# Performance work log

Measured on AMD Instinct MI355X. Metric: run time of the kernel, lower is better.

The kernel has to match this reference:

```python
import jax, jax.numpy as jnp
import numpy as np

C = 0.01          # curvature
EPS = 1e-6        # eps used in midpoint / weight normalization (matches torch code)
MIN_NORM = 1e-10  # numerical floor for norms
BALL_EPS = 1e-5   # projection margin


def _norm(x):
    return jnp.sqrt(jnp.clip(jnp.sum(x * x, axis=-1, keepdims=True), MIN_NORM))


def log_map_zero(x, c):
    sc = jnp.sqrt(c)
    n = _norm(x)
    return jnp.arctanh(jnp.clip(sc * n, -1.0 + BALL_EPS, 1.0 - BALL_EPS)) * x / (sc * n)


def exp_map_zero(v, c):
    sc = jnp.sqrt(c)
    n = _norm(v)
    return jnp.tanh(sc * n) * v / (sc * n)


def project_to_ball(x, c):
    n = _norm(x)
    maxn = (1.0 - BALL_EPS) / jnp.sqrt(c)
    return jnp.where(n > maxn, x * (maxn / n), x)


def mobius_add(x, y, c):
    x2 = jnp.sum(x * x, axis=-1, keepdims=True)
    y2 = jnp.sum(y * y, axis=-1, keepdims=True)
    xy = jnp.sum(x * y, axis=-1, keepdims=True)
    num = (1.0 + 2.0 * c * xy + c * y2) * x + (1.0 - c * x2) * y
    den = 1.0 + 2.0 * c * xy + (c * c) * x2 * y2
    return num / jnp.clip(den, MIN_NORM)


def setup_inputs() -> dict:
    N, E, R, D = 50000, 400000, 230, 16
    key = jax.random.key(0)
    ks = jax.random.split(key, 8)
    h_hyper = project_to_ball(0.1 * jax.random.normal(ks[0], (N, D), dtype=jnp.float32), C)
    node_norm = jax.random.uniform(ks[1], (N, 1), dtype=jnp.float32)
    xav = float(np.sqrt(2.0 / (D + D)))
    rel_weight = xav * jax.random.normal(ks[2], (R, D, D), dtype=jnp.float32)
    loop_weight = xav * jax.random.normal(ks[3], (D, D), dtype=jnp.float32)
    rel_emb = 0.1 * jax.random.normal(ks[4], (R, D), dtype=jnp.float32)
    src = jax.random.randint(ks[5], (E,), 0, N, dtype=jnp.int32)
    dst = jax.random.randint(ks[6], (E,), 0, N, dtype=jnp.int32)
    etype = jax.random.randint(ks[7], (E,), 0, R, dtype=jnp.int32)
    return {"h_hyper": h_hyper, "node_norm": node_norm, "rel_weight": rel_weight,
            "loop_weight": loop_weight, "rel_emb": rel_emb,
            "src": src, "dst": dst, "etype": etype}


def reference(h_hyper, node_norm, rel_weight, loop_weight, rel_emb, src, dst, etype):
    c = C
    N = h_hyper.shape[0]
    # --- msg_func: Mobius matvec per edge (log -> gathered GEMM -> +rel -> exp) ---
    h_tan = log_map_zero(h_hyper, c)                                  # [N, D]
    msg_tan = jnp.einsum('ei,eio->eo', h_tan[src], rel_weight[etype])  # [E, D]
    msg_tan = msg_tan + rel_emb[etype]
    msg = exp_map_zero(msg_tan, c)                                    # [E, D]
    # --- reduce_func: Einstein midpoint per destination node ---
    en = node_norm[dst, 0]                                            # [E] per-edge dst norm
    norm_sum = jax.ops.segment_sum(en, dst, num_segments=N)           # [N]
    w = en / (norm_sum[dst] + EPS)                                    # normalized weights
    lam = 2.0 / (1.0 - c * jnp.sum(msg * msg, axis=-1) + EPS)         # Lorentz factors [E]
    wl = w * lam
    numer = jax.ops.segment_sum(wl[:, None] * msg, dst, num_segments=N)  # [N, D]
    denom = jax.ops.segment_sum(wl, dst, num_segments=N) + EPS           # [N]
    h_agg = project_to_ball(numer / denom[:, None], c)
    # --- self loop in tangent space, combined with Mobius addition ---
    loop_hyp = exp_map_zero(h_tan @ loop_weight, c)
    h_new = mobius_add(h_agg, loop_hyp, c)
    return h_new
```

## Files before the change

### kernel.cpp

```cpp
#include <hip/hip_runtime.h>

#define C_CURV   0.01f
#define SQRT_C   0.1f
#define EPS_W    1e-6f
#define MIN_NORM 1e-10f
#define BALL_EPS 1e-5f
#define CAP      64

typedef __attribute__((ext_vector_type(4))) float f32x4;

__device__ __forceinline__ float fast_rcp(float x)  { return __builtin_amdgcn_rcpf(x); }
__device__ __forceinline__ float fast_sqrt(float x) { return __builtin_amdgcn_sqrtf(x); }
__device__ __forceinline__ float tanh_over_x(float x) {
    float t = __expf(2.0f * x);
    return (t - 1.0f) * fast_rcp((t + 1.0f) * x);
}

__device__ __forceinline__ float group4_sum(float v) {
    v += __shfl_xor(v, 1, 64);
    v += __shfl_xor(v, 2, 64);
    return v;
}

__global__ __launch_bounds__(256) void fhnn_prep(
        const float* __restrict__ h_hyper,
        const float* __restrict__ loop_weight,
        float* __restrict__ h_tan,
        float* __restrict__ loop_hyp,
        int*   __restrict__ cursor,
        int    nZero4,
        int N, int blocksN) {
    if ((int)blockIdx.x >= blocksN) {
        int i = (blockIdx.x - blocksN) * blockDim.x + threadIdx.x;
        if (i < nZero4) ((int4*)cursor)[i] = make_int4(0, 0, 0, 0);
        return;
    }
    __shared__ float Wl[256];
    Wl[threadIdx.x] = loop_weight[threadIdx.x];
    __syncthreads();

    int gid = blockIdx.x * blockDim.x + threadIdx.x;
    int t = gid >> 2, j = gid & 3;
    if (t >= N) return;

    f32x4 x = ((const f32x4*)h_hyper)[gid];

    float sq  = group4_sum(x.x * x.x + x.y * x.y + x.z * x.z + x.w * x.w);
    float n   = fast_sqrt(fmaxf(sq, MIN_NORM));
    float scn = SQRT_C * n;
    float z   = fminf(scn, 1.0f - BALL_EPS);
    float at  = 0.5f * __logf((1.0f + z) * fast_rcp(1.0f - z));
    float s   = at * fast_rcp(scn);
    f32x4 ht  = x * s;
    ((f32x4*)h_tan)[gid] = ht;

    f32x4 acc = (f32x4)(0.0f);
    #pragma unroll
    for (int q = 0; q < 4; ++q) {
        float h0 = __shfl(ht.x, q, 4);
        float h1 = __shfl(ht.y, q, 4);
        float h2 = __shfl(ht.z, q, 4);
        float h3 = __shfl(ht.w, q, 4);
        const f32x4* Wrow = (const f32x4*)Wl;
        acc += h0 * Wrow[(4 * q + 0) * 4 + j];
        acc += h1 * Wrow[(4 * q + 1) * 4 + j];
        acc += h2 * Wrow[(4 * q + 2) * 4 + j];
        acc += h3 * Wrow[(4 * q + 3) * 4 + j];
    }
    float sq2  = group4_sum(acc.x * acc.x + acc.y * acc.y + acc.z * acc.z + acc.w * acc.w);
    float n2   = fast_sqrt(fmaxf(sq2, MIN_NORM));
    float f2   = tanh_over_x(SQRT_C * n2);
    ((f32x4*)loop_hyp)[gid] = acc * f2;
}

__global__ __launch_bounds__(256) void fhnn_scatter(
        const int* __restrict__ src,
        const int* __restrict__ dst,
        const int* __restrict__ etype,
        int*      __restrict__ cursor,
        unsigned* __restrict__ bucket,
        int E) {
    int e = blockIdx.x * blockDim.x + threadIdx.x;
    if (e >= E) return;
    int t = dst[e];
    int slot = atomicAdd(&cursor[t], 1);
    if (slot < CAP)
        bucket[t * CAP + slot] = (unsigned)src[e] | ((unsigned)etype[e] << 16);
}

__global__ __launch_bounds__(256) void fhnn_reduce(
        const float*    __restrict__ h_tan,
        const float*    __restrict__ rel_weight,
        const float*    __restrict__ rel_emb,
        const unsigned* __restrict__ bucket,
        const int*      __restrict__ cursor,
        const float*    __restrict__ node_norm,
        const float*    __restrict__ loop_hyp,
        float*          __restrict__ out,
        int N) {
    int wid  = (blockIdx.x * blockDim.x + threadIdx.x) >> 6;
    int lane = threadIdx.x & 63;
    int grp  = lane >> 4;
    int slot = (lane >> 2) & 3;
    int j    = lane & 3;
    int t    = wid * 4 + grp;
    if (t >= N) return;

    int cn = min(cursor[t], CAP);

    f32x4 accM = (f32x4)(0.0f);
    float accL = 0.0f;
    for (int k = slot; k < cn; k += 4) {
        unsigned pk = bucket[t * CAP + k];
        int s = (int)(pk & 0xFFFFu);
        int r = (int)(pk >> 16);

        const f32x4* h4 = (const f32x4*)(h_tan + (size_t)s * 16);
        f32x4 h0 = h4[0], h1 = h4[1], h2 = h4[2], h3 = h4[3];

        const f32x4* W4 = (const f32x4*)(rel_weight + (size_t)r * 256);
        f32x4 a = (f32x4)(0.0f);
        a += h0.x * W4[ 0 * 4 + j];  a += h0.y * W4[ 1 * 4 + j];
        a += h0.z * W4[ 2 * 4 + j];  a += h0.w * W4[ 3 * 4 + j];
        a += h1.x * W4[ 4 * 4 + j];  a += h1.y * W4[ 5 * 4 + j];
        a += h1.z * W4[ 6 * 4 + j];  a += h1.w * W4[ 7 * 4 + j];
        a += h2.x * W4[ 8 * 4 + j];  a += h2.y * W4[ 9 * 4 + j];
        a += h2.z * W4[10 * 4 + j];  a += h2.w * W4[11 * 4 + j];
        a += h3.x * W4[12 * 4 + j];  a += h3.y * W4[13 * 4 + j];
        a += h3.z * W4[14 * 4 + j];  a += h3.w * W4[15 * 4 + j];

        f32x4 v = a + ((const f32x4*)(rel_emb + (size_t)r * 16))[j];

        float sq = group4_sum(v.x * v.x + v.y * v.y + v.z * v.z + v.w * v.w);
        float f  = tanh_over_x(SQRT_C * fast_sqrt(fmaxf(sq, MIN_NORM)));
        float m2 = f * f * sq;
        float lam = 2.0f * fast_rcp(1.0f - C_CURV * m2 + EPS_W);
        accM += v * (f * lam);
        accL += lam;
    }
    #pragma unroll
    for (int m = 4; m <= 8; m <<= 1) {
        accM.x += __shfl_xor(accM.x, m, 64);
        accM.y += __shfl_xor(accM.y, m, 64);
        accM.z += __shfl_xor(accM.z, m, 64);
        accM.w += __shfl_xor(accM.w, m, 64);
        accL   += __shfl_xor(accL,   m, 64);
    }

    float en    = node_norm[t];
    float wsc   = en * fast_rcp((float)cn * en + EPS_W);
    float denom = wsc * accL + EPS_W;
    float rs    = wsc * fast_rcp(denom);
    f32x4 x     = accM * rs;

    float x2 = group4_sum(x.x * x.x + x.y * x.y + x.z * x.z + x.w * x.w);
    float n  = fast_sqrt(fmaxf(x2, MIN_NORM));
    const float maxn = (1.0f - BALL_EPS) / SQRT_C;
    float scale = (n > maxn) ? (maxn * fast_rcp(n)) : 1.0f;
    x *= scale;

    f32x4 y   = ((const f32x4*)(loop_hyp + (size_t)t * 16))[j];
    float x2p = group4_sum(x.x * x.x + x.y * x.y + x.z * x.z + x.w * x.w);
    float y2  = group4_sum(y.x * y.x + y.y * y.y + y.z * y.z + y.w * y.w);
    float xy  = group4_sum(x.x * y.x + x.y * y.y + x.z * y.z + x.w * y.w);

    float a1  = 1.0f + 2.0f * C_CURV * xy + C_CURV * y2;
    float b1  = 1.0f - C_CURV * x2p;
    f32x4 num = a1 * x + b1 * y;
    float d2  = 1.0f + 2.0f * C_CURV * xy + C_CURV * C_CURV * x2p * y2;
    if (slot == 0)
        ((f32x4*)out)[t * 4 + j] = num * fast_rcp(fmaxf(d2, MIN_NORM));
}

extern "C" void kernel_launch(void* const* d_in, const int* in_sizes, int n_in,
                              void* d_out, int out_size, void* d_ws, size_t ws_size,
                              hipStream_t stream) {
    const float* h_hyper     = (const float*)d_in[0];
    const float* node_norm   = (const float*)d_in[1];
    const float* rel_weight  = (const float*)d_in[2];
    const float* loop_weight = (const float*)d_in[3];
    const float* rel_emb     = (const float*)d_in[4];
    const int*   src         = (const int*)d_in[5];
    const int*   dst         = (const int*)d_in[6];
    const int*   etype       = (const int*)d_in[7];

    const int N = in_sizes[1];
    const int E = in_sizes[5];

    char* ws = (char*)d_ws;
    size_t offs = 0;
    auto alloc = [&](size_t bytes) -> void* {
        void* p = ws + offs;
        offs += (bytes + 255) & ~(size_t)255;
        return p;
    };
    float*    h_tan    = (float*)alloc((size_t)N * 16 * 4);
    float*    loop_hyp = (float*)alloc((size_t)N * 16 * 4);
    unsigned* bucket   = (unsigned*)alloc((size_t)N * CAP * 4);
    int*      cursor   = (int*)alloc((size_t)N * 4);
    int nZero4 = (int)(N + 3) >> 2;

    const int threads = 256;
    int blocksN4 = (N * 4 + threads - 1) / threads;
    int blocksZ  = (nZero4 + threads - 1) / threads;
    int blocksE1 = (E + threads - 1) / threads;
    int blocksR  = (N + 15) / 16;

    fhnn_prep<<<blocksN4 + blocksZ, threads, 0, stream>>>(
        h_hyper, loop_weight, h_tan, loop_hyp, cursor, nZero4, N, blocksN4);
    fhnn_scatter<<<blocksE1, threads, 0, stream>>>(src, dst, etype, cursor, bucket, E);
    fhnn_reduce<<<blocksR, threads, 0, stream>>>(
        h_tan, rel_weight, rel_emb, bucket, cursor, node_norm, loop_hyp, (float*)d_out, N);
}
```

Measured before the change: 71.42 us.

## Stage relation weights as bf16 in LDS with persistent reduce blocks

The reduce kernel becomes persistent: 256 blocks of 1024 threads each first load all relation weights into LDS, packed as bf16 pairs with a padded stride, plus the relation embeddings. Each edge's matvec then reads weights from LDS instead of global memory. The scatter pass is folded into the prep kernel, and cursor zeroing moves to its own small kernel. The trade-offs are bf16 rounding error in the weights and a per-block staging cost of roughly 120 KB of LDS, which limits each CU to one block.

```diff
diff --git a/kernel.cpp b/kernel.cpp
--- a/kernel.cpp
+++ b/kernel.cpp
@@ -6,6 +6,7 @@
 #define MIN_NORM 1e-10f
 #define BALL_EPS 1e-5f
 #define CAP      64
+#define WSTRIDE  130
 
 typedef __attribute__((ext_vector_type(4))) float f32x4;
 
@@ -15,6 +16,10 @@
     float t = __expf(2.0f * x);
     return (t - 1.0f) * fast_rcp((t + 1.0f) * x);
 }
+__device__ __forceinline__ unsigned bf16_rne(float x) {
+    unsigned u = __float_as_uint(x);
+    return (u + 0x7FFFu + ((u >> 16) & 1u)) >> 16;
+}
 
 __device__ __forceinline__ float group4_sum(float v) {
     v += __shfl_xor(v, 1, 64);
@@ -22,17 +27,29 @@
     return v;
 }
 
+__global__ __launch_bounds__(256) void fhnn_zero(int* __restrict__ cursor, int n4) {
+    int i = blockIdx.x * blockDim.x + threadIdx.x;
+    if (i < n4) ((int4*)cursor)[i] = make_int4(0, 0, 0, 0);
+}
+
 __global__ __launch_bounds__(256) void fhnn_prep(
         const float* __restrict__ h_hyper,
         const float* __restrict__ loop_weight,
+        const int*   __restrict__ src,
+        const int*   __restrict__ dst,
+        const int*   __restrict__ etype,
         float* __restrict__ h_tan,
         float* __restrict__ loop_hyp,
-        int*   __restrict__ cursor,
-        int    nZero4,
-        int N, int blocksN) {
+        int*      __restrict__ cursor,
+        unsigned* __restrict__ bucket,
+        int N, int E, int blocksN) {
     if ((int)blockIdx.x >= blocksN) {
-        int i = (blockIdx.x - blocksN) * blockDim.x + threadIdx.x;
-        if (i < nZero4) ((int4*)cursor)[i] = make_int4(0, 0, 0, 0);
+        int e = (blockIdx.x - blocksN) * blockDim.x + threadIdx.x;
+        if (e >= E) return;
+        int t = dst[e];
+        int slot = atomicAdd(&cursor[t], 1);
+        if (slot < CAP)
+            bucket[(size_t)t * CAP + slot] = (unsigned)src[e] | ((unsigned)etype[e] << 16);
         return;
     }
     __shared__ float Wl[256];
@@ -73,22 +90,7 @@
     ((f32x4*)loop_hyp)[gid] = acc * f2;
 }
 
-__global__ __launch_bounds__(256) void fhnn_scatter(
-        const int* __restrict__ src,
-        const int* __restrict__ dst,
-        const int* __restrict__ etype,
-        int*      __restrict__ cursor,
-        unsigned* __restrict__ bucket,
-        int E) {
-    int e = blockIdx.x * blockDim.x + threadIdx.x;
-    if (e >= E) return;
-    int t = dst[e];
-    int slot = atomicAdd(&cursor[t], 1);
-    if (slot < CAP)
-        bucket[t * CAP + slot] = (unsigned)src[e] | ((unsigned)etype[e] << 16);
-}
-
-__global__ __launch_bounds__(256) void fhnn_reduce(
+__global__ __launch_bounds__(1024, 1) void fhnn_reduce(
         const float*    __restrict__ h_tan,
         const float*    __restrict__ rel_weight,
         const float*    __restrict__ rel_emb,
@@ -97,79 +99,102 @@
         const float*    __restrict__ node_norm,
         const float*    __restrict__ loop_hyp,
         float*          __restrict__ out,
-        int N) {
-    int wid  = (blockIdx.x * blockDim.x + threadIdx.x) >> 6;
+        int N, int R) {
+    extern __shared__ unsigned lds_w[];
+    const int relOff = ((R * WSTRIDE + 3) & ~3);
+    float* relE = (float*)(lds_w + relOff);
+
+    const int totalW = R * 128;
+    for (int idx = threadIdx.x; idx < totalW; idx += blockDim.x) {
+        int r = idx >> 7, c = idx & 127;
+        float a = rel_weight[r * 256 + 2 * c];
+        float b = rel_weight[r * 256 + 2 * c + 1];
+        lds_w[r * WSTRIDE + c] = bf16_rne(a) | (bf16_rne(b) << 16);
+    }
+    for (int idx = threadIdx.x; idx < R * 16; idx += blockDim.x)
+        relE[idx] = rel_emb[idx];
+    __syncthreads();
+
+    int wv   = threadIdx.x >> 6;
     int lane = threadIdx.x & 63;
     int grp  = lane >> 4;
     int slot = (lane >> 2) & 3;
     int j    = lane & 3;
-    int t    = wid * 4 + grp;
-    if (t >= N) return;
-
-    int cn = min(cursor[t], CAP);
-
-    f32x4 accM = (f32x4)(0.0f);
-    float accL = 0.0f;
-    for (int k = slot; k < cn; k += 4) {
-        unsigned pk = bucket[t * CAP + k];
-        int s = (int)(pk & 0xFFFFu);
-        int r = (int)(pk >> 16);
-
-        const f32x4* h4 = (const f32x4*)(h_tan + (size_t)s * 16);
-        f32x4 h0 = h4[0], h1 = h4[1], h2 = h4[2], h3 = h4[3];
-
-        const f32x4* W4 = (const f32x4*)(rel_weight + (size_t)r * 256);
-        f32x4 a = (f32x4)(0.0f);
-        a += h0.x * W4[ 0 * 4 + j];  a += h0.y * W4[ 1 * 4 + j];
-        a += h0.z * W4[ 2 * 4 + j];  a += h0.w * W4[ 3 * 4 + j];
-        a += h1.x * W4[ 4 * 4 + j];  a += h1.y * W4[ 5 * 4 + j];
-        a += h1.z * W4[ 6 * 4 + j];  a += h1.w * W4[ 7 * 4 + j];
-        a += h2.x * W4[ 8 * 4 + j];  a += h2.y * W4[ 9 * 4 + j];
-        a += h2.z * W4[10 * 4 + j];  a += h2.w * W4[11 * 4 + j];
-        a += h3.x * W4[12 * 4 + j];  a += h3.y * W4[13 * 4 + j];
-        a += h3.z * W4[14 * 4 + j];  a += h3.w * W4[15 * 4 + j];
-
-        f32x4 v = a + ((const f32x4*)(rel_emb + (size_t)r * 16))[j];
-
-        float sq = group4_sum(v.x * v.x + v.y * v.y + v.z * v.z + v.w * v.w);
-        float f  = tanh_over_x(SQRT_C * fast_sqrt(fmaxf(sq, MIN_NORM)));
-        float m2 = f * f * sq;
-        float lam = 2.0f * fast_rcp(1.0f - C_CURV * m2 + EPS_W);
-        accM += v * (f * lam);
-        accL += lam;
-    }
-    #pragma unroll
-    for (int m = 4; m <= 8; m <<= 1) {
-        accM.x += __shfl_xor(accM.x, m, 64);
-        accM.y += __shfl_xor(accM.y, m, 64);
-        accM.z += __shfl_xor(accM.z, m, 64);
-        accM.w += __shfl_xor(accM.w, m, 64);
-        accL   += __shfl_xor(accL,   m, 64);
-    }
-
-    float en    = node_norm[t];
-    float wsc   = en * fast_rcp((float)cn * en + EPS_W);
-    float denom = wsc * accL + EPS_W;
-    float rs    = wsc * fast_rcp(denom);
-    f32x4 x     = accM * rs;
-
-    float x2 = group4_sum(x.x * x.x + x.y * x.y + x.z * x.z + x.w * x.w);
-    float n  = fast_sqrt(fmaxf(x2, MIN_NORM));
-    const float maxn = (1.0f - BALL_EPS) / SQRT_C;
-    float scale = (n > maxn) ? (maxn * fast_rcp(n)) : 1.0f;
-    x *= scale;
-
-    f32x4 y   = ((const f32x4*)(loop_hyp + (size_t)t * 16))[j];
-    float x2p = group4_sum(x.x * x.x + x.y * x.y + x.z * x.z + x.w * x.w);
-    float y2  = group4_sum(y.x * y.x + y.y * y.y + y.z * y.z + y.w * y.w);
-    float xy  = group4_sum(x.x * y.x + x.y * y.y + x.z * y.z + x.w * y.w);
-
-    float a1  = 1.0f + 2.0f * C_CURV * xy + C_CURV * y2;
-    float b1  = 1.0f - C_CURV * x2p;
-    f32x4 num = a1 * x + b1 * y;
-    float d2  = 1.0f + 2.0f * C_CURV * xy + C_CURV * C_CURV * x2p * y2;
-    if (slot == 0)
-        ((f32x4*)out)[t * 4 + j] = num * fast_rcp(fmaxf(d2, MIN_NORM));
+
+    for (int base = blockIdx.x * 64; base < N; base += gridDim.x * 64) {
+        int t = base + wv * 4 + grp;
+        if (t >= N) continue;
+
+        int cn = min(cursor[t], CAP);
+
+        f32x4 accM = (f32x4)(0.0f);
+        float accL = 0.0f;
+        for (int k = slot; k < cn; k += 4) {
+            unsigned pk = bucket[(size_t)t * CAP + k];
+            int s = (int)(pk & 0xFFFFu);
+            int r = (int)(pk >> 16);
+
+            const f32x4* h4 = (const f32x4*)(h_tan + (size_t)s * 16);
+            f32x4 h0 = h4[0], h1 = h4[1], h2 = h4[2], h3 = h4[3];
+
+            const unsigned* Ws = lds_w + (unsigned)r * WSTRIDE + 2u * (unsigned)j;
+            f32x4 a4 = (f32x4)(0.0f);
+            #define WSTEP(HS, I) { \
+                uint2 w = *(const uint2*)(Ws + 8 * (I)); \
+                f32x4 wvv; \
+                wvv.x = __uint_as_float(w.x << 16); \
+                wvv.y = __uint_as_float(w.x & 0xFFFF0000u); \
+                wvv.z = __uint_as_float(w.y << 16); \
+                wvv.w = __uint_as_float(w.y & 0xFFFF0000u); \
+                a4 += (HS) * wvv; }
+            WSTEP(h0.x,  0) WSTEP(h0.y,  1) WSTEP(h0.z,  2) WSTEP(h0.w,  3)
+            WSTEP(h1.x,  4) WSTEP(h1.y,  5) WSTEP(h1.z,  6) WSTEP(h1.w,  7)
+            WSTEP(h2.x,  8) WSTEP(h2.y,  9) WSTEP(h2.z, 10) WSTEP(h2.w, 11)
+            WSTEP(h3.x, 12) WSTEP(h3.y, 13) WSTEP(h3.z, 14) WSTEP(h3.w, 15)
+            #undef WSTEP
+
+            f32x4 v = a4 + *(const f32x4*)(relE + r * 16 + 4 * j);
+
+            float sq = group4_sum(v.x * v.x + v.y * v.y + v.z * v.z + v.w * v.w);
+            float f  = tanh_over_x(SQRT_C * fast_sqrt(fmaxf(sq, MIN_NORM)));
+            float m2 = f * f * sq;
+            float lam = 2.0f * fast_rcp(1.0f - C_CURV * m2 + EPS_W);
+            accM += v * (f * lam);
+            accL += lam;
+        }
+        #pragma unroll
+        for (int m = 4; m <= 8; m <<= 1) {
+            accM.x += __shfl_xor(accM.x, m, 64);
+            accM.y += __shfl_xor(accM.y, m, 64);
+            accM.z += __shfl_xor(accM.z, m, 64);
+            accM.w += __shfl_xor(accM.w, m, 64);
+            accL   += __shfl_xor(accL,   m, 64);
+        }
+
+        float en    = node_norm[t];
+        float wsc   = en * fast_rcp((float)cn * en + EPS_W);
+        float denom = wsc * accL + EPS_W;
+        float rs    = wsc * fast_rcp(denom);
+        f32x4 x     = accM * rs;
+
+        float x2 = group4_sum(x.x * x.x + x.y * x.y + x.z * x.z + x.w * x.w);
+        float n  = fast_sqrt(fmaxf(x2, MIN_NORM));
+        const float maxn = (1.0f - BALL_EPS) / SQRT_C;
+        float scale = (n > maxn) ? (maxn * fast_rcp(n)) : 1.0f;
+        x *= scale;
+
+        f32x4 y   = ((const f32x4*)(loop_hyp + (size_t)t * 16))[j];
+        float x2p = group4_sum(x.x * x.x + x.y * x.y + x.z * x.z + x.w * x.w);
+        float y2  = group4_sum(y.x * y.x + y.y * y.y + y.z * y.z + y.w * y.w);
+        float xy  = group4_sum(x.x * y.x + x.y * y.y + x.z * y.z + x.w * y.w);
+
+        float a1  = 1.0f + 2.0f * C_CURV * xy + C_CURV * y2;
+        float b1  = 1.0f - C_CURV * x2p;
+        f32x4 num = a1 * x + b1 * y;
+        float d2  = 1.0f + 2.0f * C_CURV * xy + C_CURV * C_CURV * x2p * y2;
+        if (slot == 0)
+            ((f32x4*)out)[t * 4 + j] = num * fast_rcp(fmaxf(d2, MIN_NORM));
+    }
 }
 
 extern "C" void kernel_launch(void* const* d_in, const int* in_sizes, int n_in,
@@ -186,6 +211,7 @@
 
     const int N = in_sizes[1];
     const int E = in_sizes[5];
+    const int R = in_sizes[2] / 256;
 
     char* ws = (char*)d_ws;
     size_t offs = 0;
@@ -198,17 +224,24 @@
     float*    loop_hyp = (float*)alloc((size_t)N * 16 * 4);
     unsigned* bucket   = (unsigned*)alloc((size_t)N * CAP * 4);
     int*      cursor   = (int*)alloc((size_t)N * 4);
-    int nZero4 = (int)(N + 3) >> 2;
+    int nZero4 = (N + 3) >> 2;
+
+    int relOff   = ((R * WSTRIDE + 3) & ~3);
+    int ldsBytes = (relOff + R * 16) * 4;
+    hipFuncSetAttribute((const void*)fhnn_reduce,
+                        hipFuncAttributeMaxDynamicSharedMemorySize, ldsBytes);
 
     const int threads = 256;
+    int blocksZ  = (nZero4 + threads - 1) / threads;
     int blocksN4 = (N * 4 + threads - 1) / threads;
-    int blocksZ  = (nZero4 + threads - 1) / threads;
     int blocksE1 = (E + threads - 1) / threads;
-    int blocksR  = (N + 15) / 16;
-
-    fhnn_prep<<<blocksN4 + blocksZ, threads, 0, stream>>>(
-        h_hyper, loop_weight, h_tan, loop_hyp, cursor, nZero4, N, blocksN4);
-    fhnn_scatter<<<blocksE1, threads, 0, stream>>>(src, dst, etype, cursor, bucket, E);
-    fhnn_reduce<<<blocksR, threads, 0, stream>>>(
-        h_tan, rel_weight, rel_emb, bucket, cursor, node_norm, loop_hyp, (float*)d_out, N);
-}
+    int blocksR  = 256;
+
+    fhnn_zero<<<blocksZ, threads, 0, stream>>>(cursor, nZero4);
+    fhnn_prep<<<blocksN4 + blocksE1, threads, 0, stream>>>(
+        h_hyper, loop_weight, src, dst, etype, h_tan, loop_hyp, cursor, bucket,
+        N, E, blocksN4);
+    fhnn_reduce<<<blocksR, 1024, ldsBytes, stream>>>(
+        h_tan, rel_weight, rel_emb, bucket, cursor, node_norm, loop_hyp,
+        (float*)d_out, N, R);
+}
```

Result: faster. 66.65 us (-6.7%).
